# Kernel tuning notes

Hardware: AMD Instinct MI355X
Metric: run time of the kernel (lower is better)

Reference implementation:

```python
import jax, jax.numpy as jnp
import numpy as np

NEG, NEG2, EPS, K = 0.01, 0.2, 1e-5, 10
B, N = 8, 2048

def lrelu(x, s):
    return jnp.where(x >= 0, x, s * x)

def bn_eval(x, g, b):
    # BatchNorm in eval mode with running_mean=0, running_var=1
    shp = [1] * x.ndim; shp[1] = -1
    return x * (g / np.sqrt(1.0 + EPS)).reshape(shp) + b.reshape(shp)

def conv1d(x, W, b):  # x [B,C,N], W [O,C]
    return jnp.einsum('bcn,oc->bon', x, W) + b[None, :, None]

def conv2d_1x1(x, W, b):  # x [B,C,N,K], W [O,C]
    return jnp.einsum('bcnk,oc->bonk', x, W) + b[None, :, None, None]

def edge_feats(x, k):
    # x: [B, d, N] -> [B, 2d, N, k]
    xt = jnp.swapaxes(x, 1, 2)                                   # [B,N,d]
    dist = (-2.0 * jnp.einsum('bnd,bdm->bnm', xt, x)
            + jnp.sum(xt ** 2, axis=2, keepdims=True)
            + jnp.sum(x ** 2, axis=1, keepdims=True))            # [B,N,N]
    idx = jnp.argsort(dist, axis=2)[:, :, 1:k + 1]               # [B,N,k]
    nbrs = jax.vmap(lambda xb, ib: xb[:, ib])(x, idx)            # [B,d,N,k]
    c = x[:, :, :, None]
    return jnp.concatenate([jnp.broadcast_to(c, nbrs.shape), nbrs - c], axis=1)

def edge_block(x, wc1, wcb1, bn1g, bn1b, wc2, wcb2, bn2g, bn2b,
               xc, xcb, xbng, xbnb, oW, ob):
    C = x.shape[1]
    ee = edge_feats(x, K)                                        # [B,2C,N,K]
    w = lrelu(bn_eval(conv2d_1x1(ee[:, C:], wc1, wcb1), bn1g, bn1b), NEG)
    w = lrelu(bn_eval(conv2d_1x1(w, wc2, wcb2), bn2g, bn2b), NEG)
    w = jax.nn.softmax(w, axis=-1)
    h = lrelu(bn_eval(conv2d_1x1(ee, xc, xcb), xbng, xbnb), NEG)
    # Conv2d(Fout, Fout, [1,K]): contract channels and neighbor axis
    return jnp.einsum('bcnj,ocj->bon', h * w, oW) + ob[None, :, None]

def adain(x, style, W, b):
    s = conv1d(style, W, b)
    g, be = jnp.split(s, 2, axis=1)
    m = jnp.mean(x, axis=2, keepdims=True)
    v = jnp.mean((x - m) ** 2, axis=2, keepdims=True)
    return g * ((x - m) * jax.lax.rsqrt(v + EPS)) + be

def _forward(z, x, hW1, hb1, hW2, hb2,
             e1_wc1, e1_wcb1, e1_bn1g, e1_bn1b, e1_wc2, e1_wcb2, e1_bn2g, e1_bn2b,
             e1_xc, e1_xcb, e1_xbng, e1_xbnb, e1_oW, e1_ob, a1_W, a1_b,
             e2_wc1, e2_wcb1, e2_bn1g, e2_bn1b, e2_wc2, e2_wcb2, e2_bn2g, e2_bn2b,
             e2_xc, e2_xcb, e2_xbng, e2_xbnb, e2_oW, e2_ob, a2_W, a2_b,
             gW1, gb1, gbn1g, gbn1b, gW2, gb2, gbn2g, gbn2b,
             tW1, tb1, tW2, tb2, tW3, tb3):
    st = jnp.swapaxes(jnp.concatenate([x, z], axis=-1), 1, 2)    # [B,3+nz,N]
    st = lrelu(conv1d(st, hW1, hb1), NEG)
    st = lrelu(conv1d(st, hW2, hb2), NEG)                        # [B,128,N]
    pc = jnp.swapaxes(x, 1, 2)                                   # [B,3,N]
    x1 = edge_block(pc, e1_wc1, e1_wcb1, e1_bn1g, e1_bn1b, e1_wc2, e1_wcb2,
                    e1_bn2g, e1_bn2b, e1_xc, e1_xcb, e1_xbng, e1_xbnb, e1_oW, e1_ob)
    x1 = adain(lrelu(x1, NEG2), st, a1_W, a1_b)                  # [B,64,N]
    x2 = edge_block(x1, e2_wc1, e2_wcb1, e2_bn1g, e2_bn1b, e2_wc2, e2_wcb2,
                    e2_bn2g, e2_bn2b, e2_xc, e2_xcb, e2_xbng, e2_xbnb, e2_oW, e2_ob)
    x2 = adain(lrelu(x2, NEG2), st, a2_W, a2_b)                  # [B,128,N]
    fg = jnp.max(x2, axis=2)                                     # [B,128]
    fg = lrelu(bn_eval(fg @ gW1.T + gb1, gbn1g, gbn1b), NEG)
    fg = lrelu(bn_eval(fg @ gW2.T + gb2, gbn2g, gbn2b), NEG)     # [B,512]
    fg = jnp.broadcast_to(fg[:, :, None], (fg.shape[0], 512, x2.shape[2]))
    feat = jnp.concatenate([fg, x2], axis=1)                     # [B,640,N]
    t = lrelu(conv1d(feat, tW1, tb1), NEG)
    t = lrelu(conv1d(t, tW2, tb2), NEG)
    t = conv1d(t, tW3, tb3)
    return jnp.swapaxes(t, 1, 2)                                 # [B,N,3]

_PARAM_SPECS = [
    ('hW1', (128, 131)), ('hb1', (128,)), ('hW2', (128, 128)), ('hb2', (128,)),
    ('e1_wc1', (32, 3)), ('e1_wcb1', (32,)), ('e1_bn1g', (32,)), ('e1_bn1b', (32,)),
    ('e1_wc2', (64, 32)), ('e1_wcb2', (64,)), ('e1_bn2g', (64,)), ('e1_bn2b', (64,)),
    ('e1_xc', (64, 6)), ('e1_xcb', (64,)), ('e1_xbng', (64,)), ('e1_xbnb', (64,)),
    ('e1_oW', (64, 64, 10)), ('e1_ob', (64,)), ('a1_W', (128, 128)), ('a1_b', (128,)),
    ('e2_wc1', (64, 64)), ('e2_wcb1', (64,)), ('e2_bn1g', (64,)), ('e2_bn1b', (64,)),
    ('e2_wc2', (128, 64)), ('e2_wcb2', (128,)), ('e2_bn2g', (128,)), ('e2_bn2b', (128,)),
    ('e2_xc', (128, 128)), ('e2_xcb', (128,)), ('e2_xbng', (128,)), ('e2_xbnb', (128,)),
    ('e2_oW', (128, 128, 10)), ('e2_ob', (128,)), ('a2_W', (256, 128)), ('a2_b', (256,)),
    ('gW1', (128, 128)), ('gb1', (128,)), ('gbn1g', (128,)), ('gbn1b', (128,)),
    ('gW2', (512, 128)), ('gb2', (512,)), ('gbn2g', (512,)), ('gbn2b', (512,)),
    ('tW1', (256, 640)), ('tb1', (256,)), ('tW2', (64, 256)), ('tb2', (64,)),
    ('tW3', (3, 64)), ('tb3', (3,)),
]

def setup_inputs() -> dict:
    key = jax.random.key(0)
    d = {
        'z': jax.random.normal(jax.random.fold_in(key, 1000), (B, N, 128), jnp.float32),
        'x': jax.random.normal(jax.random.fold_in(key, 1001), (B, N, 3), jnp.float32),
    }
    for i, (nm, sh) in enumerate(_PARAM_SPECS):
        v = 0.1 * jax.random.normal(jax.random.fold_in(key, i), sh, jnp.float32)
        if nm.endswith('g'):  # batchnorm gammas around 1
            v = v + 1.0
        d[nm] = v
    return d

def reference(z, x, hW1, hb1, hW2, hb2,
              e1_wc1, e1_wcb1, e1_bn1g, e1_bn1b, e1_wc2, e1_wcb2, e1_bn2g, e1_bn2b,
              e1_xc, e1_xcb, e1_xbng, e1_xbnb, e1_oW, e1_ob, a1_W, a1_b,
              e2_wc1, e2_wcb1, e2_bn1g, e2_bn1b, e2_wc2, e2_wcb2, e2_bn2g, e2_bn2b,
              e2_xc, e2_xcb, e2_xbng, e2_xbnb, e2_oW, e2_ob, a2_W, a2_b,
              gW1, gb1, gbn1g, gbn1b, gW2, gb2, gbn2g, gbn2b,
              tW1, tb1, tW2, tb2, tW3, tb3):
    return _forward(z, x, hW1, hb1, hW2, hb2,
                    e1_wc1, e1_wcb1, e1_bn1g, e1_bn1b, e1_wc2, e1_wcb2, e1_bn2g, e1_bn2b,
                    e1_xc, e1_xcb, e1_xbng, e1_xbnb, e1_oW, e1_ob, a1_W, a1_b,
                    e2_wc1, e2_wcb1, e2_bn1g, e2_bn1b, e2_wc2, e2_wcb2, e2_bn2g, e2_bn2b,
                    e2_xc, e2_xcb, e2_xbng, e2_xbnb, e2_oW, e2_ob, a2_W, a2_b,
                    gW1, gb1, gbn1g, gbn1b, gW2, gb2, gbn2g, gbn2b,
                    tW1, tb1, tW2, tb2, tW3, tb3)
```

## Files before the change

### kernel.cpp

```cpp
#include <hip/hip_runtime.h>
#include <math.h>

#define NPTS 2048
#define BATCH 8
#define KNB 10
#define NT (NPTS*KNB)

static __device__ __forceinline__ float lrelu(float x, float s){ return x >= 0.f ? x : s*x; }
static __device__ __forceinline__ double lrelu_d(double x, double s){ return x >= 0.0 ? x : s*x; }

template<int TM, int TN>
__global__ __launch_bounds__(256) void gemm_bn(
    const float* __restrict__ In, int ldn, size_t inBS, int koff,
    const float* __restrict__ W, int wstride, int wcol0,
    const float* __restrict__ cb, const float* __restrict__ bng, const float* __restrict__ bnb,
    const float* __restrict__ addBO, int addM,
    float* __restrict__ Out, int ldo, size_t outBS,
    int C, int act, float neg, int bbase)
{
  constexpr int RM = TM/16, RN = TN/16;
  __shared__ float As[16][TM+4];
  __shared__ float Bs[16][TN+4];
  const int b = bbase + blockIdx.z;
  const float* in = In + (size_t)b*inBS;
  float* outp = Out + (size_t)b*outBS;
  const int m0 = blockIdx.y*TM, n0 = blockIdx.x*TN;
  const int t = threadIdx.x;
  const int tmv = t>>4, tnv = t&15;
  float acc[RM][RN] = {};
  for (int k0=0; k0<C; k0+=16){
    #pragma unroll
    for (int s=0;s<RM;s++){
      const int i = t + s*256;
      const int k = i&15, m = i>>4;
      As[k][m] = W[(size_t)(m0+m)*wstride + wcol0 + k0 + k];
    }
    #pragma unroll
    for (int s=0;s<RN;s++){
      const int i = t + s*256;
      const int n = i & (TN-1), kk2 = i / TN;
      Bs[kk2][n] = in[(size_t)(koff + k0 + kk2)*ldn + n0 + n];
    }
    __syncthreads();
    #pragma unroll
    for (int kk=0;kk<16;kk++){
      float av[RM], bv[RN];
      #pragma unroll
      for (int s=0;s<RM/4;s++){
        float4 v = *(const float4*)&As[kk][tmv*RM + s*4];
        av[s*4]=v.x; av[s*4+1]=v.y; av[s*4+2]=v.z; av[s*4+3]=v.w;
      }
      #pragma unroll
      for (int s=0;s<RN/4;s++){
        float4 v = *(const float4*)&Bs[kk][tnv*RN + s*4];
        bv[s*4]=v.x; bv[s*4+1]=v.y; bv[s*4+2]=v.z; bv[s*4+3]=v.w;
      }
      #pragma unroll
      for (int i2=0;i2<RM;i2++)
        #pragma unroll
        for (int j2=0;j2<RN;j2++) acc[i2][j2] += av[i2]*bv[j2];
    }
    __syncthreads();
  }
  const float rs = 1.f/sqrtf(1.f + 1e-5f);
  #pragma unroll
  for (int i2=0;i2<RM;i2++){
    const int gm = m0 + tmv*RM + i2;
    float addv = cb ? cb[gm] : 0.f;
    if (addBO) addv += addBO[b*addM + gm];
    float sc = 1.f, bs = 0.f;
    if (bng){ sc = bng[gm]*rs; bs = bnb[gm]; }
    float* orow = outp + (size_t)gm*ldo + n0 + tnv*RN;
    #pragma unroll
    for (int j4=0;j4<RN/4;j4++){
      float4 o;
      float vv[4];
      #pragma unroll
      for (int q=0;q<4;q++){
        float v = acc[i2][j4*4+q] + addv;
        if (bng) v = v*sc + bs;
        if (act) v = lrelu(v, neg);
        vv[q] = v;
      }
      o.x=vv[0]; o.y=vv[1]; o.z=vv[2]; o.w=vv[3];
      *(float4*)&orow[j4*4] = o;
    }
  }
}

__global__ __launch_bounds__(256) void conv_gemm_exact(
    const float* __restrict__ in, const float* __restrict__ W, int wstride, int wcol0,
    const float* __restrict__ bias,
// ... 115 lines not shown
  s = __fadd_rn(s, __fmul_rn(p[2],p[2]));
  XN[q] = s;
}

__global__ __launch_bounds__(256) void knn_part3(
    const float* __restrict__ Xn, const float* __restrict__ XN,
    double* __restrict__ topd, int* __restrict__ topi)
{
  const int t = threadIdx.x;
  const int qloc = t & 31, part = t >> 5;
  const int q = blockIdx.x*32 + qloc;
  const int b = q >> 11, n = q & (NPTS-1);
  const float* xb = Xn + (size_t)b*NPTS*3;
  const float qx = xb[(size_t)n*3+0], qy = xb[(size_t)n*3+1], qz = xb[(size_t)n*3+2];
  const float qn = XN[q];
  float td[11]; int ti[11];
  #pragma unroll
  for (int r=0;r<11;r++){ td[r] = 3.4e38f; ti[r] = 0x7fffffff; }
  const int m0 = part*(NPTS/8);
  for (int mm=0; mm<NPTS/8; mm++){
    const int m = m0 + mm;
    float dot = __fmul_rn(qx, xb[(size_t)m*3+0]);
    dot = __fadd_rn(dot, __fmul_rn(qy, xb[(size_t)m*3+1]));
    dot = __fadd_rn(dot, __fmul_rn(qz, xb[(size_t)m*3+2]));
    float dist = __fmul_rn(-2.f, dot);
    dist = __fadd_rn(dist, qn);
    dist = __fadd_rn(dist, XN[b*NPTS + m]);
    if (dist < td[10]){
      td[10] = dist; ti[10] = m;
      #pragma unroll
      for (int p=10;p>0;p--){
        if (td[p] < td[p-1]){
          float tf=td[p]; td[p]=td[p-1]; td[p-1]=tf;
          int   tt=ti[p]; ti[p]=ti[p-1]; ti[p-1]=tt;
        }
      }
    }
  }
  const size_t base = ((size_t)q*8 + part)*11;
  #pragma unroll
  for (int r=0;r<11;r++){ topd[base+r] = (double)td[r]; topi[base+r] = ti[r]; }
}

__global__ __launch_bounds__(256) void knn_merge_kernel(
    const double* __restrict__ topd, const int* __restrict__ topi, int* __restrict__ idxout)
{
  const int q = blockIdx.x*256 + threadIdx.x;
  double td[11]; int ti[11];
  #pragma unroll
  for (int r=0;r<11;r++){ td[r] = 1.0e308; ti[r] = 0x7fffffff; }
  const size_t base = (size_t)q*88;
  for (int s=0; s<88; s++){
    const double d = topd[base+s];
    const int  im = topi[base+s];
    if (d < td[10] || (d == td[10] && im < ti[10])){
      td[10] = d; ti[10] = im;
      #pragma unroll
      for (int p=10;p>0;p--){
        const bool sw = (td[p] < td[p-1]) || (td[p] == td[p-1] && ti[p] < ti[p-1]);
        if (sw){
          double tf=td[p]; td[p]=td[p-1]; td[p-1]=tf;
          int    tt=ti[p]; ti[p]=ti[p-1]; ti[p-1]=tt;
        }
      }
    }
  }
  #pragma unroll
  for (int j=0;j<KNB;j++) idxout[(size_t)q*KNB + j] = ti[j+1];
}

__global__ __launch_bounds__(256) void norms64_f32(const float* __restrict__ Xn, float* __restrict__ XN)
{
  const int q = blockIdx.x*256 + threadIdx.x;
  const float4* p4 = (const float4*)(Xn + (size_t)q*64);
  float s0=0.f,s1=0.f,s2=0.f,s3=0.f;
  #pragma unroll
  for (int d4=0; d4<16; d4++){
    float4 v = p4[d4];
    s0 += v.x*v.x; s1 += v.y*v.y; s2 += v.z*v.z; s3 += v.w*v.w;
  }
  XN[q] = (s0+s1)+(s2+s3);
}

__global__ __launch_bounds__(256) void knn_coarse(
    const float* __restrict__ Xn, const float* __restrict__ XN,
    float* __restrict__ topf, int* __restrict__ topi)
{
  const int t = threadIdx.x;
  const int qloc = t & 31, part = t >> 5;
  const int q = blockIdx.x*32 + qloc;
  const int b = q >> 11, n = q & (NPTS-1);
  const float* xb = Xn + (size_t)b*NPTS*64;
  float qv[64];
  {
    const float4* p4 = (const float4*)(xb + (size_t)n*64);
    #pragma unroll
    for (int d4=0; d4<16; d4++){ float4 v = p4[d4]; qv[d4*4]=v.x; qv[d4*4+1]=v.y; qv[d4*4+2]=v.z; qv[d4*4+3]=v.w; }
  }
  const float qn = XN[q];
  float td[16]; int ti[16];
  #pragma unroll
  for (int r=0;r<16;r++){ td[r] = 3.4e38f; ti[r] = 0x7fffffff; }
  const int m0 = part*(NPTS/8);
  for (int mm=0; mm<NPTS/8; mm++){
    const int m = m0 + mm;
    const float4* c4 = (const float4*)(xb + (size_t)m*64);
    float d0=0.f,d1=0.f,d2=0.f,d3=0.f;
    #pragma unroll
    for (int d4=0; d4<16; d4++){
      float4 v = c4[d4];
      d0 += qv[d4*4+0]*v.x; d1 += qv[d4*4+1]*v.y;
      d2 += qv[d4*4+2]*v.z; d3 += qv[d4*4+3]*v.w;
    }
    const float dist = qn - 2.f*((d0+d1)+(d2+d3)) + XN[b*NPTS + m];
    if (dist < td[15]){
      td[15] = dist; ti[15] = m;
      #pragma unroll
      for (int p=15;p>0;p--){
        if (td[p] < td[p-1]){
          float tf=td[p]; td[p]=td[p-1]; td[p-1]=tf;
          int   tt=ti[p]; ti[p]=ti[p-1]; ti[p-1]=tt;
        }
      }
    }
  }
  const size_t base = ((size_t)q*8 + part)*16;
  #pragma unroll
  for (int r=0;r<16;r++){ topf[base+r] = td[r]; topi[base+r] = ti[r]; }
}

__global__ __launch_bounds__(256) void knn_refine(
    const float* __restrict__ topf, const int* __restrict__ topi,
    const double* __restrict__ Xd, const double* __restrict__ XNd,
    int* __restrict__ idxout)
{
  const int q = blockIdx.x*256 + threadIdx.x;
  const int b = q >> 11;
  float tf[16]; int ti[16];
  #pragma unroll
  for (int r=0;r<16;r++){ tf[r] = 3.4e38f; ti[r] = 0x7fffffff; }
  const size_t base = (size_t)q*128;
  for (int s=0; s<128; s++){
    const float d = topf[base+s];
    const int  im = topi[base+s];
    if (d < tf[15] || (d == tf[15] && im < ti[15])){
      tf[15] = d; ti[15] = im;
      #pragma unroll
      for (int p=15;p>0;p--){
        const bool sw = (tf[p] < tf[p-1]) || (tf[p] == tf[p-1] && ti[p] < ti[p-1]);
        if (sw){
          float a=tf[p]; tf[p]=tf[p-1]; tf[p-1]=a;
          int   c=ti[p]; ti[p]=ti[p-1]; ti[p-1]=c;
        }
      }
    }
  }
  double qv[64];
  {
    const double2* p2 = (const double2*)(Xd + (size_t)q*64);
    #pragma unroll
    for (int d2=0; d2<32; d2++){ double2 v = p2[d2]; qv[d2*2]=v.x; qv[d2*2+1]=v.y; }
  }
  const double qn = XNd[q];
  double dd[11]; int di[11];
  #pragma unroll
  for (int r=0;r<11;r++){ dd[r] = 1.0e308; di[r] = 0x7fffffff; }
  for (int s=0; s<16; s++){
    const int m = ti[s];
    const double2* c2 = (const double2*)(Xd + ((size_t)(b*NPTS + m))*64);
    double d0=0.0,d1=0.0,d2s=0.0,d3=0.0;
    #pragma unroll
    for (int d4=0; d4<16; d4++){
      double2 va = c2[d4*2], vb = c2[d4*2+1];
      d0 += qv[d4*4+0]*va.x; d1 += qv[d4*4+1]*va.y;
      d2s+= qv[d4*4+2]*vb.x; d3 += qv[d4*4+3]*vb.y;
    }
    const double dot = (d0+d1)+(d2s+d3);
    const double dist = (qn - 2.0*dot) + XNd[b*NPTS + m];
    if (dist < dd[10] || (dist == dd[10] && m < di[10])){
      dd[10] = dist; di[10] = m;
      #pragma unroll
      for (int p=10;p>0;p--){
        const bool sw = (dd[p] < dd[p-1]) || (dd[p] == dd[p-1] && di[p] < di[p-1]);
        if (sw){
          double a=dd[p]; dd[p]=dd[p-1]; dd[p-1]=a;
          int    c=di[p]; di[p]=di[p-1]; di[p-1]=c;
        }
      }
    }
  }
  #pragma unroll
  for (int j=0;j<KNB;j++) idxout[(size_t)q*KNB + j] = di[j+1];
}

__global__ __launch_bounds__(512) void edge1_f64(
    const float* __restrict__ Xn, const int* __restrict__ idx,
    const float* __restrict__ wc1, const float* __restrict__ wcb1,
    const float* __restrict__ bn1g, const float* __restrict__ bn1b,
    const float* __restrict__ wc2, const float* __restrict__ wcb2,
    const float* __restrict__ bn2g, const float* __restrict__ bn2b,
    const float* __restrict__ xc,  const float* __restrict__ xcb,
    const float* __restrict__ xbng, const float* __restrict__ xbnb,
    const float* __restrict__ oWT, const float* __restrict__ ob,
    double* __restrict__ outX)
{
  __shared__ float wc1s[32][3];
  __shared__ float wc2s[64][33];
  __shared__ float xcs[64][7];
  __shared__ float wcb1s[32], wcb2s[64], xcbs[64];
  __shared__ double fs1d[32], fb1d[32], fs2d[64], fb2d[64], fsxd[64], fbxd[64];
  __shared__ float cenb[8][3], difb[8][3];
  __shared__ double w1bd[8][32];
  __shared__ float smw2[4096];
  __shared__ double hwbd[8][64];

  const int t = threadIdx.x;
  const double sq = sqrt(1.0 + 1e-5);
  for (int i=t; i<96;   i+=512) wc1s[i/3][i%3] = wc1[i];
  for (int i=t; i<2048; i+=512) wc2s[i/32][i%32] = wc2[i];
  for (int i=t; i<384;  i+=512) xcs[i/6][i%6] = xc[i];
  if (t < 32){ wcb1s[t]=wcb1[t]; fs1d[t]=(double)bn1g[t]/sq; fb1d[t]=(double)bn1b[t]; }
  else if (t < 96){ int o=t-32; wcb2s[o]=wcb2[o]; fs2d[o]=(double)bn2g[o]/sq; fb2d[o]=(double)bn2b[o]; }
  else if (t < 160){ int o=t-96; xcbs[o]=xcb[o]; fsxd[o]=(double)xbng[o]/sq; fbxd[o]=(double)xbnb[o]; }
  __syncthreads();

  const int wid = t>>6, lane = t&63;
  const int p = blockIdx.x*8 + wid;
  const int b = p >> 11, n = p & (NPTS-1);
  const float* xb = Xn + (size_t)b*NPTS*3;
  if (lane < 3) cenb[wid][lane] = xb[(size_t)n*3 + lane];
  __builtin_amdgcn_wave_barrier();
  const int* ip = idx + ((size_t)b*NPTS + n)*KNB;

  double w2r[KNB], hr[KNB];
  #pragma unroll
  for (int j=0;j<KNB;j++){
    const int id = ip[j];
    if (lane < 3) difb[wid][lane] = __fadd_rn(xb[(size_t)id*3 + lane], -cenb[wid][lane]);
// ... 167 lines not shown
      }
    }
    __syncthreads();
  }
  #pragma unroll
  for (int i2=0;i2<4;i2++){
    const int m = tm*4 + i2;
    #pragma unroll
    for (int j=0;j<8;j++){
      const int n = n0 + tn + j*16;
      if (y == 0) WCC[((size_t)b*64 + m)*NPTS + n] = acc[i2][j];
      else        HCC[((size_t)b*128 + (y-1)*64 + m)*NPTS + n] = acc[i2][j];
    }
  }
}

__global__ __launch_bounds__(256) void kernelA(
    const float* __restrict__ X1f, const int* __restrict__ IDX,
    const float* __restrict__ WCC,
    const float* __restrict__ wc1, const float* __restrict__ wcb1,
    const float* __restrict__ bn1g, const float* __restrict__ bn1b,
    float* __restrict__ W1, int bbase)
{
  __shared__ float wc1T[64*68];
  __shared__ float nbr[64*132];
  __shared__ int idx_l[128];
  const int b = bbase + blockIdx.z;
  const int n0 = blockIdx.x*128;
  const int t = threadIdx.x;
  const float* xb = X1f + (size_t)b*NPTS*64;

  if (t < 128){
    const int n = n0 + t;
    idx_l[t] = IDX[((size_t)b*NPTS + n/10)*KNB + (n%10)];
  }
  for (int i=t; i<4096; i+=256){
    const int k = i&63, m = i>>6;
    wc1T[k*68 + m] = wc1[(size_t)m*64 + k];
  }
  __syncthreads();
  const float4* xb4 = (const float4*)xb;
  #pragma unroll
  for (int r=0; r<8; r++){
    const int i = t + r*256;
    const int pos = i>>4, q4 = i&15;
    const float4 v = xb4[(size_t)idx_l[pos]*16 + q4];
    nbr[(q4*4+0)*132 + pos] = v.x;
    nbr[(q4*4+1)*132 + pos] = v.y;
    nbr[(q4*4+2)*132 + pos] = v.z;
    nbr[(q4*4+3)*132 + pos] = v.w;
  }
  __syncthreads();

  const int tm = t>>4, tn = t&15;
  float acc[4][8] = {};
  #pragma unroll 4
  for (int k=0;k<64;k++){
    float4 a4 = *(const float4*)&wc1T[k*68 + tm*4];
    const float av[4] = {a4.x, a4.y, a4.z, a4.w};
    #pragma unroll
    for (int j=0;j<8;j++){
      const float bv = nbr[k*132 + tn + j*16];
      #pragma unroll
      for (int i2=0;i2<4;i2++) acc[i2][j] += av[i2]*bv;
    }
  }
  const float rs = 1.f/sqrtf(1.f + 1e-5f);
  #pragma unroll
  for (int i2=0;i2<4;i2++){
    const int m = tm*4 + i2;
    const float bias = wcb1[m];
    const float sc = bn1g[m]*rs, bb = bn1b[m];
    #pragma unroll
    for (int j=0;j<8;j++){
      const int n = n0 + tn + j*16;
      const int p = n/10;
      float v = acc[i2][j] - WCC[((size_t)b*64 + m)*NPTS + p] + bias;
      v = lrelu(v*sc + bb, 0.01f);
      W1[((size_t)(b-bbase)*64 + m)*NT + n] = v;
    }
  }
}

#define SM_WC2T 0
#define SM_XCDT 8448
#define SM_W1S  16896
#define SM_NBRS 22144
#define SM_TOT  27392
#define SM_HW   0
#define SM_OWL  10304

__global__ __launch_bounds__(256) void kernelC(
    const float* __restrict__ X1f, const int* __restrict__ IDX,
    const float* __restrict__ W1, const float* __restrict__ HCC,
    const float* __restrict__ wc2, const float* __restrict__ wcb2,
    const float* __restrict__ bn2g, const float* __restrict__ bn2b,
    const float* __restrict__ xc,  const float* __restrict__ xcb,
    const float* __restrict__ xbng, const float* __restrict__ xbnb,
    const float* __restrict__ oW, const float* __restrict__ ob,
    float* __restrict__ X2, int bbase)
{
  __shared__ float smC[SM_TOT];
  __shared__ int idxC[80];
  const int b = bbase + blockIdx.z;
  const int n0 = blockIdx.x*80;
  const int p0 = n0/10;
  const int t = threadIdx.x;
  const float* xb = X1f + (size_t)b*NPTS*64;

  if (t < 80){
    const int n = n0 + t;
    idxC[t] = IDX[((size_t)b*NPTS + n/10)*KNB + (n%10)];
  }
  for (int i=t; i<8192; i+=256){
    const int k = i&63, c = i>>6;
    smC[SM_WC2T + k*132 + c] = wc2[(size_t)c*64 + k];
    smC[SM_XCDT + k*132 + c] = xc[(size_t)c*128 + 64 + k];
  }
  for (int i=t; i<5120; i+=256){
    const int n = i%80, k = i/80;
    smC[SM_W1S + k*82 + n] = W1[((size_t)(b-bbase)*64 + k)*NT + n0 + n];
  }
  __syncthreads();
  {
    const float4* xb4 = (const float4*)xb;
    #pragma unroll
    for (int r=0; r<5; r++){
      const int i = t + r*256;
      const int pos = i>>4, q4 = i&15;
      const float4 v = xb4[(size_t)idxC[pos]*16 + q4];
      smC[SM_NBRS + (q4*4+0)*82 + pos] = v.x;
      smC[SM_NBRS + (q4*4+1)*82 + pos] = v.y;
      smC[SM_NBRS + (q4*4+2)*82 + pos] = v.z;
      smC[SM_NBRS + (q4*4+3)*82 + pos] = v.w;
    }
  }
  __syncthreads();

  const int tmv = t>>4;
  const int tnv = t&15;
  const int tnv5 = tnv*5;
  float accw[8][5] = {};
  float acch[8][5] = {};
  #pragma unroll 2
  for (int k=0;k<64;k++){
    float av[8], xv[8];
    {
      float4 v0 = *(const float4*)&smC[SM_WC2T + k*132 + tmv*8];
      float4 v1 = *(const float4*)&smC[SM_WC2T + k*132 + tmv*8 + 4];
      av[0]=v0.x; av[1]=v0.y; av[2]=v0.z; av[3]=v0.w;
      av[4]=v1.x; av[5]=v1.y; av[6]=v1.z; av[7]=v1.w;
      float4 w0 = *(const float4*)&smC[SM_XCDT + k*132 + tmv*8];
      float4 w1v= *(const float4*)&smC[SM_XCDT + k*132 + tmv*8 + 4];
      xv[0]=w0.x; xv[1]=w0.y; xv[2]=w0.z; xv[3]=w0.w;
      xv[4]=w1v.x; xv[5]=w1v.y; xv[6]=w1v.z; xv[7]=w1v.w;
    }
    float bw[5], bh[5];
    #pragma unroll
    for (int j=0;j<5;j++){
      bw[j] = smC[SM_W1S  + k*82 + tnv5 + j];
      bh[j] = smC[SM_NBRS + k*82 + tnv5 + j];
    }
    #pragma unroll
    for (int i2=0;i2<8;i2++)
      #pragma unroll
      for (int j=0;j<5;j++){
        accw[i2][j] += av[i2]*bw[j];
        acch[i2][j] += xv[i2]*bh[j];
      }
  }

  const float rs = 1.f/sqrtf(1.f + 1e-5f);
  const int p_loc = tnv>>1;
  float hwreg[8][5];
  #pragma unroll
  for (int i2=0;i2<8;i2++){
    const int c = tmv*8 + i2;
    const float s2 = bn2g[c]*rs, b2 = bn2b[c], cb2 = wcb2[c];
    const float sx = xbng[c]*rs, bx = xbnb[c], cbx = xcb[c];
    const float hcc = HCC[((size_t)b*128 + c)*NPTS + p0 + p_loc];
    float w2[5], hv[5];
    #pragma unroll
    for (int j=0;j<5;j++){
      w2[j] = lrelu((accw[i2][j] + cb2)*s2 + b2, 0.01f);
      hv[j] = lrelu((acch[i2][j] + hcc + cbx)*sx + bx, 0.01f);
    }
    float mx = w2[0];
    #pragma unroll
    for (int j=1;j<5;j++) mx = fmaxf(mx, w2[j]);
    mx = fmaxf(mx, __shfl_xor(mx, 1));
    float ssum = 0.f;
    #pragma unroll
    for (int j=0;j<5;j++){ w2[j] = expf(w2[j]-mx); ssum += w2[j]; }
    ssum += __shfl_xor(ssum, 1);
    const float inv = 1.f/ssum;
    #pragma unroll
    for (int j=0;j<5;j++) hwreg[i2][j] = hv[j]*(w2[j]*inv);
  }
  __syncthreads();

  {
    const int jh5 = (tnv&1)*5;
    #pragma unroll
    for (int i2=0;i2<8;i2++){
      const int c = tmv*8 + i2;
      #pragma unroll
      for (int j=0;j<5;j++)
        smC[SM_HW + p_loc*1288 + c*10 + jh5 + j] = hwreg[i2][j];
    }
  }
  __syncthreads();

  const int o = t & 127;
  const int phalf = t >> 7;
  float acc2[4] = {};
  for (int kc=0; kc<1280; kc+=64){
    __syncthreads();
    #pragma unroll
    for (int r=0;r<32;r++){
      const int i = t + r*256;
      const int oo = i>>6, kk = i&63;
      smC[SM_OWL + oo*65 + kk] = oW[(size_t)oo*1280 + kc + kk];
    }
    __syncthreads();
    #pragma unroll 4
    for (int kk=0; kk<64; kk+=4){
      const float w0 = smC[SM_OWL + o*65 + kk];
      const float w1v= smC[SM_OWL + o*65 + kk+1];
      const float w2v= smC[SM_OWL + o*65 + kk+2];
      const float w3v= smC[SM_OWL + o*65 + kk+3];
      #pragma unroll
      for (int pp=0;pp<4;pp++){
        const float4 h4 = *(const float4*)&smC[SM_HW + (phalf*4+pp)*1288 + kc + kk];
        acc2[pp] += w0*h4.x + w1v*h4.y + w2v*h4.z + w3v*h4.w;
      }
    }
  }
  const float obv = ob[o];
  #pragma unroll
  for (int pp=0;pp<4;pp++)
    X2[((size_t)b*128 + o)*NPTS + p0 + phalf*4 + pp] = acc2[pp] + obv;
}

template<int CH>
__global__ __launch_bounds__(256) void adain_kernel(
    float* __restrict__ X, const float* __restrict__ S)
{
  const int c = blockIdx.x, b = blockIdx.y;
  const int t = threadIdx.x;
  const size_t base = ((size_t)b*CH + c)*NPTS;
  __shared__ float red[256];
  float v[8];
  float s = 0.f;
  #pragma unroll
  for (int i=0;i<8;i++){
    float xv = X[base + t + i*256];
    xv = lrelu(xv, 0.2f);
    v[i] = xv; s += xv;
  }
  red[t] = s; __syncthreads();
  for (int st=128; st>0; st>>=1){ if (t<st) red[t] += red[t+st]; __syncthreads(); }
  const float mean = red[0]*(1.f/NPTS);
  __syncthreads();
  float s2 = 0.f;
  #pragma unroll
  for (int i=0;i<8;i++){ const float d = v[i]-mean; s2 += d*d; }
  red[t] = s2; __syncthreads();
  for (int st=128; st>0; st>>=1){ if (t<st) red[t] += red[t+st]; __syncthreads(); }
  const float var  = red[0]*(1.f/NPTS);
  const float rstd = 1.f/sqrtf(var + 1e-5f);
  const float* g  = S + ((size_t)b*2*CH + c)*NPTS;
  const float* be = S + ((size_t)b*2*CH + CH + c)*NPTS;
  #pragma unroll
  for (int i=0;i<8;i++){
    const int n = t + i*256;
    X[base+n] = g[n]*((v[i]-mean)*rstd) + be[n];
  }
}

__global__ __launch_bounds__(256) void maxn_kernel(const float* __restrict__ X, float* __restrict__ FG)
{
  const int c = blockIdx.x, b = blockIdx.y;
  const int t = threadIdx.x;
  const float* p = X + ((size_t)b*128 + c)*NPTS;
  __shared__ float red[256];
  float m = -3.4e38f;
  for (int i=t; i<NPTS; i+=256) m = fmaxf(m, p[i]);
  red[t] = m; __syncthreads();
  for (int st=128; st>0; st>>=1){ if (t<st) red[t] = fmaxf(red[t], red[t+st]); __syncthreads(); }
  if (t == 0) FG[b*128+c] = red[0];
}

__global__ __launch_bounds__(512) void fc_kernel(
    const float* __restrict__ FG,
    const float* __restrict__ gW1, const float* __restrict__ gb1,
    const float* __restrict__ gbn1g, const float* __restrict__ gbn1b,
    const float* __restrict__ gW2, const float* __restrict__ gb2,
    const float* __restrict__ gbn2g, const float* __restrict__ gbn2b,
    const float* __restrict__ tW1, const float* __restrict__ tb1,
    float* __restrict__ FGP)
{
  const int b = blockIdx.x, t = threadIdx.x;
  __shared__ float fg[128], h1[128], h2[512];
  const float rs = 1.f/sqrtf(1.f + 1e-5f);
  if (t < 128) fg[t] = FG[b*128+t];
  __syncthreads();
  if (t < 128){
    float s = 0.f;
    for (int c=0;c<128;c++) s += gW1[t*128+c]*fg[c];
    s += gb1[t];
    s = s*(gbn1g[t]*rs) + gbn1b[t];
    h1[t] = lrelu(s, 0.01f);
  }
  __syncthreads();
  {
    float s = 0.f;
    for (int c=0;c<128;c++) s += gW2[t*128+c]*h1[c];
    s += gb2[t];
// ... 50 lines not shown
  const float* e1_xcb = (const float*)d_in[15];
  const float* e1_xbng= (const float*)d_in[16];
  const float* e1_xbnb= (const float*)d_in[17];
  const float* e1_oW  = (const float*)d_in[18];
  const float* e1_ob  = (const float*)d_in[19];
  const float* a1_W   = (const float*)d_in[20];
  const float* a1_b   = (const float*)d_in[21];
  const float* e2_wc1 = (const float*)d_in[22];
  const float* e2_wcb1= (const float*)d_in[23];
  const float* e2_bn1g= (const float*)d_in[24];
  const float* e2_bn1b= (const float*)d_in[25];
  const float* e2_wc2 = (const float*)d_in[26];
  const float* e2_wcb2= (const float*)d_in[27];
  const float* e2_bn2g= (const float*)d_in[28];
  const float* e2_bn2b= (const float*)d_in[29];
  const float* e2_xc  = (const float*)d_in[30];
  const float* e2_xcb = (const float*)d_in[31];
  const float* e2_xbng= (const float*)d_in[32];
  const float* e2_xbnb= (const float*)d_in[33];
  const float* e2_oW  = (const float*)d_in[34];
  const float* e2_ob  = (const float*)d_in[35];
  const float* a2_W   = (const float*)d_in[36];
  const float* a2_b   = (const float*)d_in[37];
  const float* gW1    = (const float*)d_in[38];
  const float* gb1    = (const float*)d_in[39];
  const float* gbn1g  = (const float*)d_in[40];
  const float* gbn1b  = (const float*)d_in[41];
  const float* gW2    = (const float*)d_in[42];
  const float* gb2    = (const float*)d_in[43];
  const float* gbn2g  = (const float*)d_in[44];
  const float* gbn2b  = (const float*)d_in[45];
  const float* tW1    = (const float*)d_in[46];
  const float* tb1    = (const float*)d_in[47];
  const float* tW2    = (const float*)d_in[48];
  const float* tb2    = (const float*)d_in[49];
  const float* tW3    = (const float*)d_in[50];
  const float* tb3    = (const float*)d_in[51];
  float* out = (float*)d_out;
  float* ws  = (float*)d_ws;

  size_t off = 0;
  float*  ST    = ws + off; off += (size_t)BATCH*128*NPTS;
  float*  Sbuf  = ws + off; off += (size_t)BATCH*256*NPTS;
  float*  X1f   = ws + off; off += (size_t)BATCH*NPTS*64;
  float*  X2    = ws + off; off += (size_t)BATCH*128*NPTS;
  float*  T1    = ws + off; off += (size_t)BATCH*256*NPTS;
  float*  T2    = ws + off; off += (size_t)BATCH*64*NPTS;
  int*    IDX   = (int*)(ws + off); off += (size_t)BATCH*NPTS*KNB;
  float*  OW1T  = ws + off; off += (size_t)64*64*KNB;
  float*  XN3f  = ws + off; off += (size_t)BATCH*NPTS;
  double* XN64  = (double*)(ws + off); off += (size_t)2*BATCH*NPTS;
  float*  FG    = ws + off; off += (size_t)BATCH*128;
  float*  FGP   = ws + off; off += (size_t)BATCH*256;
  off = (off + 1) & ~(size_t)1;
  double* X1_64 = (double*)(ws + off); off += (size_t)2*BATCH*64*NPTS;
  double* X1T64 = (double*)(ws + off); off += (size_t)2*BATCH*NPTS*64;

  double* TOPD  = (double*)T1;
  int*    TOPI  = (int*)Sbuf;
  float*  TOPF  = (float*)X1_64;
  int*    TOPI2 = (int*)T1;
  float*  X1c   = Sbuf;
  float*  WCC   = Sbuf + 1048576;
  float*  HCC   = Sbuf + 2097152;
  float*  W1    = T1;

  owt_kernel<64><<<(64*64*KNB+255)/256, 256, 0, stream>>>(e1_oW, OW1T);

  head1_exact<<<dim3(32,2,8), 256, 0, stream>>>(x, z, hW1, hb1, T1);
  conv_gemm_exact<<<dim3(32,2,8), 256, 0, stream>>>(T1, hW2, 128, 0, hb2, ST, 128, 128, 1, 0.01f);

  norms3_f32<<<64, 256, 0, stream>>>(x, XN3f);
  knn_part3<<<512, 256, 0, stream>>>(x, XN3f, TOPD, TOPI);
  knn_merge_kernel<<<64, 256, 0, stream>>>(TOPD, TOPI, IDX);
  edge1_f64<<<2048, 512, 0, stream>>>(
      x, IDX, e1_wc1, e1_wcb1, e1_bn1g, e1_bn1b, e1_wc2, e1_wcb2, e1_bn2g, e1_bn2b,
      e1_xc, e1_xcb, e1_xbng, e1_xbnb, OW1T, e1_ob, X1_64);
  conv_gemm_exact<<<dim3(32,2,8), 256, 0, stream>>>(ST, a1_W, 128, 0, a1_b, Sbuf, 128, 128, 0, 0.f);
  adain1_f64<<<dim3(64,8), 256, 0, stream>>>(X1_64, Sbuf);

  transpose_cast64<<<dim3(32,8), 256, 0, stream>>>(X1_64, X1T64, X1f, X1c);

  norms64_f32<<<64, 256, 0, stream>>>(X1f, XN3f);
  norms64d_label:
  {
  }
  {
  }
  extern __global__ void norms64d(const double*, double*);
  norms64d<<<64, 256, 0, stream>>>(X1T64, XN64);
  knn_coarse<<<512, 256, 0, stream>>>(X1f, XN3f, TOPF, TOPI2);
  knn_refine<<<64, 256, 0, stream>>>(TOPF, TOPI2, X1T64, XN64, IDX);

  kernelP<<<dim3(16,3,8), 256, 0, stream>>>(X1c, e2_wc1, e2_xc, WCC, HCC);
  for (int lb=0; lb<4; lb++){
    const int bbase = lb*2;
    kernelA<<<dim3(NT/128,1,2), 256, 0, stream>>>(
        X1f, IDX, WCC, e2_wc1, e2_wcb1, e2_bn1g, e2_bn1b, W1, bbase);
    kernelC<<<dim3(NT/80,1,2), 256, 0, stream>>>(
        X1f, IDX, W1, HCC, e2_wc2, e2_wcb2, e2_bn2g, e2_bn2b,
        e2_xc, e2_xcb, e2_xbng, e2_xbnb, e2_oW, e2_ob, X2, bbase);
  }

  gemm_bn<128,128><<<dim3(NPTS/128,2,8), 256, 0, stream>>>(
      ST, NPTS, (size_t)128*NPTS, 0, a2_W, 128, 0, a2_b, nullptr, nullptr, nullptr, 0,
      Sbuf, NPTS, (size_t)256*NPTS, 128, 0, 0.f, 0);
  adain_kernel<128><<<dim3(128,8), 256, 0, stream>>>(X2, Sbuf);

  maxn_kernel<<<dim3(128,8), 256, 0, stream>>>(X2, FG);
  fc_kernel<<<8, 512, 0, stream>>>(FG, gW1, gb1, gbn1g, gbn1b, gW2, gb2, gbn2g, gbn2b, tW1, tb1, FGP);
  gemm_bn<128,128><<<dim3(NPTS/128,2,8), 256, 0, stream>>>(
      X2, NPTS, (size_t)128*NPTS, 0, tW1, 640, 512, nullptr, nullptr, nullptr, FGP, 256,
      T1, NPTS, (size_t)256*NPTS, 128, 1, 0.01f, 0);
  gemm_bn<64,128><<<dim3(NPTS/128,1,8), 256, 0, stream>>>(
      T1, NPTS, (size_t)256*NPTS, 0, tW2, 256, 0, tb2, nullptr, nullptr, nullptr, 0,
      T2, NPTS, (size_t)64*NPTS, 256, 1, 0.01f, 0);
  t3_kernel<<<dim3(8,8), 256, 0, stream>>>(T2, tW3, tb3, out);
}

__global__ __launch_bounds__(256) void norms64d(const double* __restrict__ Xn, double* __restrict__ XN)
{
  const int q = blockIdx.x*256 + threadIdx.x;
  const double* p = Xn + (size_t)q*64;
  double s = 0.0;
  #pragma unroll
  for (int d=0; d<64; d++) s += p[d]*p[d];
  XN[q] = s;
}
```

Measured before the change: 1.809 ms.

## Tile kNN distance search through shared memory and split kernelC channels in halves

The coarse kNN kernel becomes a shared-memory tiled GEMM. Query and candidate blocks are staged in LDS, and each thread computes 8 candidate distances per tile before inserting them into its top-16 list. Before, each thread streamed 64-float candidate rows straight from global memory. kernelC now processes its 128 output channels in two 64-channel halves, which shrinks its LDS footprint and per-thread accumulators and should allow more resident blocks. The cost is reloading the W1 tile and the neighbor gather twice, plus extra barriers.

```diff
diff --git a/kernel.cpp b/kernel.cpp
--- a/kernel.cpp
+++ b/kernel.cpp
@@ -8,6 +8,20 @@
 
 static __device__ __forceinline__ float lrelu(float x, float s){ return x >= 0.f ? x : s*x; }
 static __device__ __forceinline__ double lrelu_d(double x, double s){ return x >= 0.0 ? x : s*x; }
+
+static __device__ __forceinline__ void ins16(float d, int m, float* td, int* ti){
+  if (d < td[15] || (d == td[15] && m < ti[15])){
+    td[15] = d; ti[15] = m;
+    #pragma unroll
+    for (int p=15;p>0;p--){
+      const bool sw = (td[p] < td[p-1]) || (td[p] == td[p-1] && ti[p] < ti[p-1]);
+      if (sw){
+        float a=td[p]; td[p]=td[p-1]; td[p-1]=a;
+        int   c=ti[p]; ti[p]=ti[p-1]; ti[p-1]=c;
+      }
+    }
+  }
+}
 
 template<int TM, int TN>
 __global__ __launch_bounds__(256) void gemm_bn(
@@ -289,51 +303,67 @@
   XN[q] = (s0+s1)+(s2+s3);
 }
 
-__global__ __launch_bounds__(256) void knn_coarse(
+__global__ __launch_bounds__(256) void knn_gemm(
     const float* __restrict__ Xn, const float* __restrict__ XN,
     float* __restrict__ topf, int* __restrict__ topi)
 {
-  const int t = threadIdx.x;
-  const int qloc = t & 31, part = t >> 5;
-  const int q = blockIdx.x*32 + qloc;
-  const int b = q >> 11, n = q & (NPTS-1);
+  __shared__ float Qs[64][34];
+  __shared__ float Cs[64][68];
+  __shared__ float xns[64];
+  const int t = threadIdx.x;
+  const int q0 = blockIdx.x*32;
+  const int b  = q0 >> 11;
+  const int qloc0 = q0 & (NPTS-1);
   const float* xb = Xn + (size_t)b*NPTS*64;
-  float qv[64];
-  {
-    const float4* p4 = (const float4*)(xb + (size_t)n*64);
-    #pragma unroll
-    for (int d4=0; d4<16; d4++){ float4 v = p4[d4]; qv[d4*4]=v.x; qv[d4*4+1]=v.y; qv[d4*4+2]=v.z; qv[d4*4+3]=v.w; }
-  }
-  const float qn = XN[q];
+  for (int i=t; i<512; i+=256){
+    const int q = i>>4, f4 = i&15;
+    float4 v = *(const float4*)(xb + (size_t)(qloc0+q)*64 + f4*4);
+    Qs[f4*4+0][q]=v.x; Qs[f4*4+1][q]=v.y; Qs[f4*4+2][q]=v.z; Qs[f4*4+3][q]=v.w;
+  }
+  const int tq = t>>3, tm = t&7;
+  const int gq = q0 + tq;
+  const float qn = XN[gq];
   float td[16]; int ti[16];
   #pragma unroll
-  for (int r=0;r<16;r++){ td[r] = 3.4e38f; ti[r] = 0x7fffffff; }
-  const int m0 = part*(NPTS/8);
-  for (int mm=0; mm<NPTS/8; mm++){
-    const int m = m0 + mm;
-    const float4* c4 = (const float4*)(xb + (size_t)m*64);
-    float d0=0.f,d1=0.f,d2=0.f,d3=0.f;
-    #pragma unroll
-    for (int d4=0; d4<16; d4++){
-      float4 v = c4[d4];
-      d0 += qv[d4*4+0]*v.x; d1 += qv[d4*4+1]*v.y;
-      d2 += qv[d4*4+2]*v.z; d3 += qv[d4*4+3]*v.w;
-    }
-    const float dist = qn - 2.f*((d0+d1)+(d2+d3)) + XN[b*NPTS + m];
-    if (dist < td[15]){
-      td[15] = dist; ti[15] = m;
-      #pragma unroll
-      for (int p=15;p>0;p--){
-        if (td[p] < td[p-1]){
-          float tf=td[p]; td[p]=td[p-1]; td[p-1]=tf;
-          int   tt=ti[p]; ti[p]=ti[p-1]; ti[p-1]=tt;
-        }
-      }
-    }
-  }
-  const size_t base = ((size_t)q*8 + part)*16;
-  #pragma unroll
-  for (int r=0;r<16;r++){ topf[base+r] = td[r]; topi[base+r] = ti[r]; }
+  for (int r=0;r<16;r++){ td[r]=3.4e38f; ti[r]=0x7fffffff; }
+  for (int m0=0; m0<NPTS; m0+=64){
+    __syncthreads();
+    for (int i=t; i<1024; i+=256){
+      const int m = i>>4, f4 = i&15;
+      float4 v = *(const float4*)(xb + (size_t)(m0+m)*64 + f4*4);
+      Cs[f4*4+0][m]=v.x; Cs[f4*4+1][m]=v.y; Cs[f4*4+2][m]=v.z; Cs[f4*4+3][m]=v.w;
+    }
+    if (t < 64) xns[t] = XN[b*NPTS + m0 + t];
+    __syncthreads();
+    float acc[8] = {};
+    #pragma unroll 4
+    for (int k=0;k<64;k++){
+      const float a = Qs[k][tq];
+      float4 c0 = *(const float4*)&Cs[k][tm*8];
+      float4 c1 = *(const float4*)&Cs[k][tm*8+4];
+      acc[0]+=a*c0.x; acc[1]+=a*c0.y; acc[2]+=a*c0.z; acc[3]+=a*c0.w;
+      acc[4]+=a*c1.x; acc[5]+=a*c1.y; acc[6]+=a*c1.z; acc[7]+=a*c1.w;
+    }
+    #pragma unroll
+    for (int j=0;j<8;j++){
+      const int m = m0 + tm*8 + j;
+      const float d = qn - 2.f*acc[j] + xns[tm*8+j];
+      ins16(d, m, td, ti);
+    }
+  }
+  const size_t base = ((size_t)gq*8 + tm)*16;
+  #pragma unroll
+  for (int r=0;r<16;r++){ topf[base+r]=td[r]; topi[base+r]=ti[r]; }
+}
+
+__global__ __launch_bounds__(256) void norms64d(const double* __restrict__ Xn, double* __restrict__ XN)
+{
+  const int q = blockIdx.x*256 + threadIdx.x;
+  const double* p = Xn + (size_t)q*64;
+  double s = 0.0;
+  #pragma unroll
+  for (int d=0; d<64; d++) s += p[d]*p[d];
+  XN[q] = s;
 }
 
 __global__ __launch_bounds__(256) void knn_refine(
@@ -348,19 +378,7 @@
   for (int r=0;r<16;r++){ tf[r] = 3.4e38f; ti[r] = 0x7fffffff; }
   const size_t base = (size_t)q*128;
   for (int s=0; s<128; s++){
-    const float d = topf[base+s];
-    const int  im = topi[base+s];
-    if (d < tf[15] || (d == tf[15] && im < ti[15])){
-      tf[15] = d; ti[15] = im;
-      #pragma unroll
-      for (int p=15;p>0;p--){
-        const bool sw = (tf[p] < tf[p-1]) || (tf[p] == tf[p-1] && ti[p] < ti[p-1]);
-        if (sw){
-          float a=tf[p]; tf[p]=tf[p-1]; tf[p-1]=a;
-          int   c=ti[p]; ti[p]=ti[p-1]; ti[p-1]=c;
-        }
-      }
-    }
+    ins16(topf[base+s], topi[base+s], tf, ti);
   }
   double qv[64];
   {
@@ -694,13 +712,13 @@
   }
 }
 
-#define SM_WC2T 0
-#define SM_XCDT 8448
-#define SM_W1S  16896
-#define SM_NBRS 22144
-#define SM_TOT  27392
-#define SM_HW   0
-#define SM_OWL  10304
+#define C_WC2T 0
+#define C_XCDT 4352
+#define C_W1S  8704
+#define C_NBRS 13952
+#define C_TOT  19200
+#define C_HW   0
+#define C_OWL  5184
 
 __global__ __launch_bounds__(256) void kernelC(
     const float* __restrict__ X1f, const int* __restrict__ IDX,
@@ -712,7 +730,7 @@
     const float* __restrict__ oW, const float* __restrict__ ob,
     float* __restrict__ X2, int bbase)
 {
-  __shared__ float smC[SM_TOT];
+  __shared__ float smC[C_TOT];
   __shared__ int idxC[80];
   const int b = bbase + blockIdx.z;
   const int n0 = blockIdx.x*80;
@@ -724,128 +742,115 @@
     const int n = n0 + t;
     idxC[t] = IDX[((size_t)b*NPTS + n/10)*KNB + (n%10)];
   }
-  for (int i=t; i<8192; i+=256){
-    const int k = i&63, c = i>>6;
-    smC[SM_WC2T + k*132 + c] = wc2[(size_t)c*64 + k];
-    smC[SM_XCDT + k*132 + c] = xc[(size_t)c*128 + 64 + k];
-  }
-  for (int i=t; i<5120; i+=256){
-    const int n = i%80, k = i/80;
-    smC[SM_W1S + k*82 + n] = W1[((size_t)(b-bbase)*64 + k)*NT + n0 + n];
-  }
   __syncthreads();
-  {
-    const float4* xb4 = (const float4*)xb;
-    #pragma unroll
-    for (int r=0; r<5; r++){
-      const int i = t + r*256;
-      const int pos = i>>4, q4 = i&15;
-      const float4 v = xb4[(size_t)idxC[pos]*16 + q4];
-      smC[SM_NBRS + (q4*4+0)*82 + pos] = v.x;
-      smC[SM_NBRS + (q4*4+1)*82 + pos] = v.y;
-      smC[SM_NBRS + (q4*4+2)*82 + pos] = v.z;
-      smC[SM_NBRS + (q4*4+3)*82 + pos] = v.w;
-    }
-  }
-  __syncthreads();
-
-  const int tmv = t>>4;
-  const int tnv = t&15;
-  const int tnv5 = tnv*5;
-  float accw[8][5] = {};
-  float acch[8][5] = {};
-  #pragma unroll 2
-  for (int k=0;k<64;k++){
-    float av[8], xv[8];
+
+  const int tmv = t>>4, tnv = t&15, tnv5 = tnv*5;
+  const int p_loc = tnv>>1, jh5 = (tnv&1)*5;
+  const int o = t&127, phalf = t>>7;
+  const float rs = 1.f/sqrtf(1.f + 1e-5f);
+  float acc2[4] = {};
+
+  for (int ch=0; ch<2; ch++){
+    for (int i=t; i<4096; i+=256){
+      const int k = i&63, cl = i>>6;
+      smC[C_WC2T + k*68 + cl] = wc2[(size_t)(ch*64+cl)*64 + k];
+      smC[C_XCDT + k*68 + cl] = xc[(size_t)(ch*64+cl)*128 + 64 + k];
+    }
+    for (int i=t; i<5120; i+=256){
+      const int n = i%80, k = i/80;
+      smC[C_W1S + k*82 + n] = W1[((size_t)(b-bbase)*64 + k)*NT + n0 + n];
+    }
     {
-      float4 v0 = *(const float4*)&smC[SM_WC2T + k*132 + tmv*8];
-      float4 v1 = *(const float4*)&smC[SM_WC2T + k*132 + tmv*8 + 4];
-      av[0]=v0.x; av[1]=v0.y; av[2]=v0.z; av[3]=v0.w;
-      av[4]=v1.x; av[5]=v1.y; av[6]=v1.z; av[7]=v1.w;
-      float4 w0 = *(const float4*)&smC[SM_XCDT + k*132 + tmv*8];
-      float4 w1v= *(const float4*)&smC[SM_XCDT + k*132 + tmv*8 + 4];
-      xv[0]=w0.x; xv[1]=w0.y; xv[2]=w0.z; xv[3]=w0.w;
-      xv[4]=w1v.x; xv[5]=w1v.y; xv[6]=w1v.z; xv[7]=w1v.w;
-    }
-    float bw[5], bh[5];
-    #pragma unroll
-    for (int j=0;j<5;j++){
-      bw[j] = smC[SM_W1S  + k*82 + tnv5 + j];
-      bh[j] = smC[SM_NBRS + k*82 + tnv5 + j];
-    }
-    #pragma unroll
-    for (int i2=0;i2<8;i2++)
+      const float4* xb4 = (const float4*)xb;
+      #pragma unroll
+      for (int r=0;r<5;r++){
+        const int i = t + r*256;
+        const int pos = i>>4, q4 = i&15;
+        const float4 v = xb4[(size_t)idxC[pos]*16 + q4];
+        smC[C_NBRS + (q4*4+0)*82 + pos] = v.x;
+        smC[C_NBRS + (q4*4+1)*82 + pos] = v.y;
+        smC[C_NBRS + (q4*4+2)*82 + pos] = v.z;
+        smC[C_NBRS + (q4*4+3)*82 + pos] = v.w;
+      }
+    }
+    __syncthreads();
+
+    float accw[4][5] = {}, acch[4][5] = {};
+    #pragma unroll 2
+    for (int k=0;k<64;k++){
+      float4 a4 = *(const float4*)&smC[C_WC2T + k*68 + tmv*4];
+      float4 x4 = *(const float4*)&smC[C_XCDT + k*68 + tmv*4];
+      const float av[4] = {a4.x,a4.y,a4.z,a4.w};
+      const float xv[4] = {x4.x,x4.y,x4.z,x4.w};
+      float bw[5], bh[5];
       #pragma unroll
       for (int j=0;j<5;j++){
-        accw[i2][j] += av[i2]*bw[j];
-        acch[i2][j] += xv[i2]*bh[j];
-      }
-  }
-
-  const float rs = 1.f/sqrtf(1.f + 1e-5f);
-  const int p_loc = tnv>>1;
-  float hwreg[8][5];
-  #pragma unroll
-  for (int i2=0;i2<8;i2++){
-    const int c = tmv*8 + i2;
-    const float s2 = bn2g[c]*rs, b2 = bn2b[c], cb2 = wcb2[c];
-    const float sx = xbng[c]*rs, bx = xbnb[c], cbx = xcb[c];
-    const float hcc = HCC[((size_t)b*128 + c)*NPTS + p0 + p_loc];
-    float w2[5], hv[5];
-    #pragma unroll
-    for (int j=0;j<5;j++){
-      w2[j] = lrelu((accw[i2][j] + cb2)*s2 + b2, 0.01f);
-      hv[j] = lrelu((acch[i2][j] + hcc + cbx)*sx + bx, 0.01f);
-    }
-    float mx = w2[0];
-    #pragma unroll
-    for (int j=1;j<5;j++) mx = fmaxf(mx, w2[j]);
-    mx = fmaxf(mx, __shfl_xor(mx, 1));
-    float ssum = 0.f;
-    #pragma unroll
-    for (int j=0;j<5;j++){ w2[j] = expf(w2[j]-mx); ssum += w2[j]; }
-    ssum += __shfl_xor(ssum, 1);
-    const float inv = 1.f/ssum;
-    #pragma unroll
-    for (int j=0;j<5;j++) hwreg[i2][j] = hv[j]*(w2[j]*inv);
-  }
-  __syncthreads();
-
-  {
-    const int jh5 = (tnv&1)*5;
-    #pragma unroll
-    for (int i2=0;i2<8;i2++){
-      const int c = tmv*8 + i2;
+        bw[j] = smC[C_W1S  + k*82 + tnv5 + j];
+        bh[j] = smC[C_NBRS + k*82 + tnv5 + j];
+      }
+      #pragma unroll
+      for (int i2=0;i2<4;i2++)
+        #pragma unroll
+        for (int j=0;j<5;j++){ accw[i2][j]+=av[i2]*bw[j]; acch[i2][j]+=xv[i2]*bh[j]; }
+    }
+
+    float hwreg[4][5];
+    #pragma unroll
+    for (int i2=0;i2<4;i2++){
+      const int c = ch*64 + tmv*4 + i2;
+      const float s2 = bn2g[c]*rs, b2 = bn2b[c], cb2 = wcb2[c];
+      const float sx = xbng[c]*rs, bx = xbnb[c], cbx = xcb[c];
+      const float hcc = HCC[((size_t)b*128 + c)*NPTS + p0 + p_loc];
+      float w2[5], hv[5];
+      #pragma unroll
+      for (int j=0;j<5;j++){
+        w2[j] = lrelu((accw[i2][j] + cb2)*s2 + b2, 0.01f);
+        hv[j] = lrelu((acch[i2][j] + hcc + cbx)*sx + bx, 0.01f);
+      }
+      float mx = w2[0];
+      #pragma unroll
+      for (int j=1;j<5;j++) mx = fmaxf(mx, w2[j]);
+      mx = fmaxf(mx, __shfl_xor(mx, 1));
+      float ssum = 0.f;
+      #pragma unroll
+      for (int j=0;j<5;j++){ w2[j] = expf(w2[j]-mx); ssum += w2[j]; }
+      ssum += __shfl_xor(ssum, 1);
+      const float inv = 1.f/ssum;
+      #pragma unroll
+      for (int j=0;j<5;j++) hwreg[i2][j] = hv[j]*(w2[j]*inv);
+    }
+    __syncthreads();
+
+    #pragma unroll
+    for (int i2=0;i2<4;i2++){
+      const int cl = tmv*4 + i2;
       #pragma unroll
       for (int j=0;j<5;j++)
-        smC[SM_HW + p_loc*1288 + c*10 + jh5 + j] = hwreg[i2][j];
-    }
-  }
-  __syncthreads();
-
-  const int o = t & 127;
-  const int phalf = t >> 7;
-  float acc2[4] = {};
-  for (int kc=0; kc<1280; kc+=64){
-    __syncthreads();
-    #pragma unroll
-    for (int r=0;r<32;r++){
-      const int i = t + r*256;
-      const int oo = i>>6, kk = i&63;
-      smC[SM_OWL + oo*65 + kk] = oW[(size_t)oo*1280 + kc + kk];
-    }
-    __syncthreads();
-    #pragma unroll 4
-    for (int kk=0; kk<64; kk+=4){
-      const float w0 = smC[SM_OWL + o*65 + kk];
-      const float w1v= smC[SM_OWL + o*65 + kk+1];
-      const float w2v= smC[SM_OWL + o*65 + kk+2];
-      const float w3v= smC[SM_OWL + o*65 + kk+3];
-      #pragma unroll
-      for (int pp=0;pp<4;pp++){
-        const float4 h4 = *(const float4*)&smC[SM_HW + (phalf*4+pp)*1288 + kc + kk];
-        acc2[pp] += w0*h4.x + w1v*h4.y + w2v*h4.z + w3v*h4.w;
-      }
+        smC[C_HW + p_loc*648 + cl*10 + jh5 + j] = hwreg[i2][j];
+    }
+    __syncthreads();
+
+    for (int kc=0; kc<640; kc+=64){
+      #pragma unroll
+      for (int r=0;r<32;r++){
+        const int i = t + r*256;
+        const int oo = i>>6, kk = i&63;
+        smC[C_OWL + oo*65 + kk] = oW[(size_t)oo*1280 + ch*640 + kc + kk];
+      }
+      __syncthreads();
+      #pragma unroll 4
+      for (int kk=0; kk<64; kk+=4){
+        const float w0 = smC[C_OWL + o*65 + kk];
+        const float w1v= smC[C_OWL + o*65 + kk+1];
+        const float w2v= smC[C_OWL + o*65 + kk+2];
+        const float w3v= smC[C_OWL + o*65 + kk+3];
+        #pragma unroll
+        for (int pp=0;pp<4;pp++){
+          const float4 h4 = *(const float4*)&smC[C_HW + (phalf*4+pp)*648 + kc + kk];
+          acc2[pp] += w0*h4.x + w1v*h4.y + w2v*h4.z + w3v*h4.w;
+        }
+      }
+      __syncthreads();
     }
   }
   const float obv = ob[o];
@@ -1062,14 +1067,8 @@
   transpose_cast64<<<dim3(32,8), 256, 0, stream>>>(X1_64, X1T64, X1f, X1c);
 
   norms64_f32<<<64, 256, 0, stream>>>(X1f, XN3f);
-  norms64d_label:
-  {
-  }
-  {
-  }
-  extern __global__ void norms64d(const double*, double*);
   norms64d<<<64, 256, 0, stream>>>(X1T64, XN64);
-  knn_coarse<<<512, 256, 0, stream>>>(X1f, XN3f, TOPF, TOPI2);
+  knn_gemm<<<512, 256, 0, stream>>>(X1f, XN3f, TOPF, TOPI2);
   knn_refine<<<64, 256, 0, stream>>>(TOPF, TOPI2, X1T64, XN64, IDX);
 
   kernelP<<<dim3(16,3,8), 256, 0, stream>>>(X1c, e2_wc1, e2_xc, WCC, HCC);
@@ -1097,13 +1096,3 @@
       T2, NPTS, (size_t)64*NPTS, 256, 1, 0.01f, 0);
   t3_kernel<<<dim3(8,8), 256, 0, stream>>>(T2, tW3, tb3, out);
 }
-
-__global__ __launch_bounds__(256) void norms64d(const double* __restrict__ Xn, double* __restrict__ XN)
-{
-  const int q = blockIdx.x*256 + threadIdx.x;
-  const double* p = Xn + (size_t)q*64;
-  double s = 0.0;
-  #pragma unroll
-  for (int d=0; d<64; d++) s += p[d]*p[d];
-  XN[q] = s;
-}
```

Measured after the change: 3.374 ms. +86.5%, slower.
